# Performance work log

Measured on AMD Instinct MI355X. Metric: run time of the kernel, lower is better.

The kernel has to match this reference:

```python
import jax, jax.numpy as jnp
import numpy as np

NUM_HEADS = 16


def setup_inputs() -> dict:
    key = jax.random.key(0)
    k1, k2, k3 = jax.random.split(key, 3)
    B, N, C = 8, 1024, 1024
    x = jax.random.normal(k1, (B, N, C), dtype=jnp.float32)
    w_qkv = jax.random.normal(k2, (C, 3 * C), dtype=jnp.float32) * (C ** -0.5)
    w_proj = jax.random.normal(k3, (C, C), dtype=jnp.float32) * (C ** -0.5)
    b_proj = jnp.zeros((C,), dtype=jnp.float32)
    return {"x": x, "w_qkv": w_qkv, "w_proj": w_proj, "b_proj": b_proj}


def reference(x, w_qkv, w_proj, b_proj):
    B, N, C = x.shape
    H = NUM_HEADS
    hd = C // H
    scale = hd ** -0.5
    # qkv: [B,N,3C] -> [3,B,H,N,hd]
    qkv = (x @ w_qkv).reshape(B, N, 3, H, hd)
    qkv = jnp.transpose(qkv, (2, 0, 3, 1, 4))
    q, k, v = qkv[0], qkv[1], qkv[2]
    # attention scores [B,H,N,N], softmax over keys (attn_drop=0 in eval)
    attn = jax.nn.softmax(jnp.einsum('bhnd,bhmd->bhnm', q, k) * scale, axis=-1)
    # context -> [B,N,C]
    out = jnp.einsum('bhnm,bhmd->bnhd', attn, v).reshape(B, N, C)
    out = out @ w_proj + b_proj  # proj_drop=0 in eval
    return out, attn
```

## Files before the change

kernel.cpp:

```cpp
#include <hip/hip_runtime.h>


typedef unsigned short ushort_t;
typedef __bf16 bf16x8 __attribute__((ext_vector_type(8)));
typedef float floatx4 __attribute__((ext_vector_type(4)));

__device__ __forceinline__ ushort_t f2bf(float f) {
    __bf16 h = (__bf16)f;
    return *(ushort_t*)&h;
}

__global__ void transpose_f32_bf16(const float* __restrict__ in, ushort_t* __restrict__ out,
                                   int rows, int cols) {
    __shared__ ushort_t tile[32][33];
    int bx = blockIdx.x * 32;
    int by = blockIdx.y * 32;
    int tx = threadIdx.x;
    for (int i = threadIdx.y; i < 32; i += 8)
        tile[i][tx] = f2bf(in[(long)(by + i) * cols + bx + tx]);
    __syncthreads();
    for (int i = threadIdx.y; i < 32; i += 8)
        out[(long)(bx + i) * rows + by + tx] = tile[tx][i];
}

template <int AFP32>
__device__ __forceinline__ bf16x8 load_a8(const void* A_, long off) {
    if (AFP32) {
        const float* p = (const float*)A_ + off;
        floatx4 f0 = *(const floatx4*)p;
        floatx4 f1 = *(const floatx4*)(p + 4);
        bf16x8 r;
#pragma unroll
        for (int i = 0; i < 4; i++) { r[i] = (__bf16)f0[i]; r[i + 4] = (__bf16)f1[i]; }
        return r;
    } else {
        return *(const bf16x8*)((const ushort_t*)A_ + off);
    }
}

template <int MODE, int AFP32>
__global__ __launch_bounds__(256, 3)
void gemm_bt(const void* __restrict__ A, const ushort_t* __restrict__ Bt,
             int M, int Nc, int K,
             void* __restrict__ out_p, const float* __restrict__ bias) {
    __shared__ ushort_t As[128 * 32];
    __shared__ ushort_t Bs[128 * 32];
    const int tid  = threadIdx.x;
    const int wave = tid >> 6, lane = tid & 63;
    const int quad = lane >> 4, l16 = lane & 15;
    const int bm = blockIdx.y * 128, bn = blockIdx.x * 128;
    const int wm = (wave & 1) * 64, wn = (wave >> 1) * 64;

    floatx4 acc[4][4] = {};

    const int c0 = tid, c1 = tid + 256;
    const int row0 = c0 >> 2, kk0 = (c0 & 3) * 8;
    const int row1 = c1 >> 2, kk1 = (c1 & 3) * 8;

    for (int k0 = 0; k0 < K; k0 += 32) {
        bf16x8 a0 = load_a8<AFP32>(A, (long)(bm + row0) * K + k0 + kk0);
        bf16x8 a1 = load_a8<AFP32>(A, (long)(bm + row1) * K + k0 + kk1);
        bf16x8 b0 = *(const bf16x8*)(Bt + (long)(bn + row0) * K + k0 + kk0);
        bf16x8 b1 = *(const bf16x8*)(Bt + (long)(bn + row1) * K + k0 + kk1);
        __syncthreads();
        *(bf16x8*)&As[c0 * 8] = a0;
        *(bf16x8*)&As[c1 * 8] = a1;
        *(bf16x8*)&Bs[c0 * 8] = b0;
        *(bf16x8*)&Bs[c1 * 8] = b1;
        __syncthreads();
        bf16x8 af[4], bfr[4];
#pragma unroll
        for (int i = 0; i < 4; i++) {
            af[i]  = *(const bf16x8*)&As[(wm + i * 16 + l16) * 32 + quad * 8];
            bfr[i] = *(const bf16x8*)&Bs[(wn + i * 16 + l16) * 32 + quad * 8];
        }
#pragma unroll
        for (int mi = 0; mi < 4; mi++)
#pragma unroll
            for (int ni = 0; ni < 4; ni++)
                acc[mi][ni] = __builtin_amdgcn_mfma_f32_16x16x32_bf16(af[mi], bfr[ni], acc[mi][ni], 0, 0, 0);
    }

    if (MODE == 0) {
        ushort_t* qb  = (ushort_t*)out_p;
        ushort_t* kb  = qb + (size_t)8388608;
        ushort_t* vtb = qb + (size_t)16777216;
#pragma unroll
        for (int ni = 0; ni < 4; ni++) {
            int n = bn + wn + ni * 16 + l16;
            int t = n >> 10, c = n & 1023, h = c >> 6, d = c & 63;
#pragma unroll
            for (int mi = 0; mi < 4; mi++) {
                floatx4 v = acc[mi][ni];
#pragma unroll
                for (int r = 0; r < 4; r++) {
                    int m = bm + wm + mi * 16 + quad * 4 + r;
                    int b = m >> 10, tok = m & 1023;
                    long bh = (long)b * 16 + h;
                    ushort_t val = f2bf(v[r]);
                    if (t == 0)      qb[(bh * 1024 + tok) * 64 + d] = val;
                    else if (t == 1) kb[(bh * 1024 + tok) * 64 + d] = val;
                    else             vtb[(bh * 64 + d) * 1024 + tok] = val;
                }
            }
        }
    } else {
        float* outf = (float*)out_p;
#pragma unroll
        for (int ni = 0; ni < 4; ni++) {
            int n = bn + wn + ni * 16 + l16;
            float bv = bias[n];
#pragma unroll
            for (int mi = 0; mi < 4; mi++) {
                floatx4 v = acc[mi][ni];
#pragma unroll
                for (int r = 0; r < 4; r++) {
                    int m = bm + wm + mi * 16 + quad * 4 + r;
                    outf[(long)m * Nc + n] = v[r] + bv;
                }
            }
        }
    }
}

__global__ __launch_bounds__(256, 2)
void attn_fused(const ushort_t* __restrict__ q, const ushort_t* __restrict__ k,
                const ushort_t* __restrict__ vt, float* __restrict__ attn_out,
                ushort_t* __restrict__ ctx) {
    constexpr int SSTR = 1028;
    __shared__ float S[16 * SSTR];
    __shared__ float red_m[16];
    __shared__ float red_il[16];

    const int bh = blockIdx.x >> 6;
    const int qt = blockIdx.x & 63;
    const int qbase = qt * 16;
    const int tid = threadIdx.x;
    const int wave = tid >> 6, lane = tid & 63;
    const int quad = lane >> 4, l16 = lane & 15;

    const ushort_t* qrow = q + ((long)bh * 1024 + qbase + l16) * 64 + quad * 8;
    bf16x8 aq0 = *(const bf16x8*)(qrow);
    bf16x8 aq1 = *(const bf16x8*)(qrow + 32);

    const int key0 = wave * 256;
    const ushort_t* kp = k + ((long)bh * 1024 + key0 + l16) * 64 + quad * 8;
    bf16x8 bk0 = *(const bf16x8*)(kp);
    bf16x8 bk1 = *(const bf16x8*)(kp + 32);

    for (int kt = 0; kt < 16; kt++) {
        int ktn = (kt + 1 < 16) ? kt + 1 : 15;
        const ushort_t* npk = kp + (long)ktn * 1024;
        bf16x8 nb0 = *(const bf16x8*)(npk);
        bf16x8 nb1 = *(const bf16x8*)(npk + 32);
        floatx4 s4 = {0.f, 0.f, 0.f, 0.f};
        s4 = __builtin_amdgcn_mfma_f32_16x16x32_bf16(aq0, bk0, s4, 0, 0, 0);
        s4 = __builtin_amdgcn_mfma_f32_16x16x32_bf16(aq1, bk1, s4, 0, 0, 0);
        int keyc = key0 + kt * 16 + l16;
#pragma unroll
        for (int r = 0; r < 4; r++)
            S[(quad * 4 + r) * SSTR + keyc] = s4[r] * 0.125f;
        bk0 = nb0; bk1 = nb1;
    }
    __syncthreads();

    {
        int row = tid >> 4, sub = tid & 15;
        float m = -1e30f;
        for (int i = sub; i < 1024; i += 16) m = fmaxf(m, S[row * SSTR + i]);
#pragma unroll
        for (int o = 1; o < 16; o <<= 1) m = fmaxf(m, __shfl_xor(m, o, 64));
        float l = 0.f;
        for (int i = sub; i < 1024; i += 16) l += __expf(S[row * SSTR + i] - m);
#pragma unroll
        for (int o = 1; o < 16; o <<= 1) l += __shfl_xor(l, o, 64);
        if (sub == 0) { red_m[row] = m; red_il[row] = 1.0f / l; }
    }
    __syncthreads();

    float* aout = attn_out + ((long)bh * 1024 + qbase) * 1024;
    for (int idx = tid; idx < 16 * 256; idx += 256) {
        int r = idx >> 8, k4 = (idx & 255) * 4;
        float m = red_m[r], il = red_il[r];
        floatx4 pv;
#pragma unroll
        for (int j = 0; j < 4; j++) {
            float p = __expf(S[r * SSTR + k4 + j] - m) * il;
            S[r * SSTR + k4 + j] = p;
            pv[j] = p;
        }
        *(floatx4*)&aout[(long)r * 1024 + k4] = pv;
    }
    __syncthreads();

    floatx4 o4 = {0.f, 0.f, 0.f, 0.f};
    const ushort_t* vrow = vt + ((long)bh * 64 + wave * 16 + l16) * 1024 + quad * 8;
    for (int ks = 0; ks < 32; ks++) {
        const float* sp = &S[l16 * SSTR + ks * 32 + quad * 8];
        floatx4 p0 = *(const floatx4*)(sp);
        floatx4 p1 = *(const floatx4*)(sp + 4);
        bf16x8 pa;
#pragma unroll
        for (int i = 0; i < 4; i++) { pa[i] = (__bf16)p0[i]; pa[i + 4] = (__bf16)p1[i]; }
        bf16x8 vb = *(const bf16x8*)(vrow + ks * 32);
        o4 = __builtin_amdgcn_mfma_f32_16x16x32_bf16(pa, vb, o4, 0, 0, 0);
    }
    int b = bh >> 4, h = bh & 15;
    ushort_t* cp = ctx + ((long)b * 1024 + qbase) * 1024 + h * 64 + wave * 16 + l16;
#pragma unroll
    for (int r = 0; r < 4; r++)
        cp[(long)(quad * 4 + r) * 1024] = f2bf(o4[r]);
}

extern "C" void kernel_launch(void* const* d_in, const int* in_sizes, int n_in,
                              void* d_out, int out_size, void* d_ws, size_t ws_size,
                              hipStream_t stream) {
    const float* x      = (const float*)d_in[0];
    const float* w_qkv  = (const float*)d_in[1];
    const float* w_proj = (const float*)d_in[2];
    const float* b_proj = (const float*)d_in[3];

    float* out  = (float*)d_out;
    float* attn = out + (size_t)8 * 1024 * 1024;

    ushort_t* ws     = (ushort_t*)d_ws;
    ushort_t* q      = ws;
    ushort_t* kk     = ws + (size_t)8  * 1024 * 1024;
    ushort_t* vt     = ws + (size_t)16 * 1024 * 1024;
    ushort_t* ctx    = ws + (size_t)24 * 1024 * 1024;
    ushort_t* wqkvt  = ws + (size_t)32 * 1024 * 1024;
    ushort_t* wprojt = ws + (size_t)35 * 1024 * 1024;

    transpose_f32_bf16<<<dim3(96, 32), dim3(32, 8), 0, stream>>>(w_qkv, wqkvt, 1024, 3072);
    transpose_f32_bf16<<<dim3(32, 32), dim3(32, 8), 0, stream>>>(w_proj, wprojt, 1024, 1024);

    gemm_bt<0, 1><<<dim3(24, 64), dim3(256), 0, stream>>>(x, wqkvt, 8192, 3072, 1024, q, (const float*)nullptr);

    attn_fused<<<dim3(8192), dim3(256), 0, stream>>>(q, kk, vt, attn, ctx);

    gemm_bt<1, 0><<<dim3(8, 64), dim3(256), 0, stream>>>(ctx, wprojt, 8192, 1024, 1024, out, b_proj);
}
```

Baseline: 991.6 us.

## Keep attention scores in registers and stage probabilities as swizzled bf16 in LDS

The score tile now stays in registers, with the softmax max and sum computed through lane shuffles and a small cross-wave LDS reduction. This replaces the 64KB fp32 shared buffer and its multiple passes. Probabilities are written to LDS as bf16 with an XOR swizzle, which shrinks LDS use so the launch bound can rise to 3 blocks per SM. The catch is that the global attn stores become scalar per-lane writes instead of float4 vectors, and holding 16 floatx4 per lane raises register pressure.

```diff
diff --git a/kernel.cpp b/kernel.cpp
--- a/kernel.cpp
+++ b/kernel.cpp
@@ -123,14 +123,13 @@
     }
 }
 
-__global__ __launch_bounds__(256, 2)
+__global__ __launch_bounds__(256, 3)
 void attn_fused(const ushort_t* __restrict__ q, const ushort_t* __restrict__ k,
                 const ushort_t* __restrict__ vt, float* __restrict__ attn_out,
                 ushort_t* __restrict__ ctx) {
-    constexpr int SSTR = 1028;
-    __shared__ float S[16 * SSTR];
-    __shared__ float red_m[16];
-    __shared__ float red_il[16];
+    __shared__ ushort_t Sb[16 * 1024];
+    __shared__ float redm[4][16];
+    __shared__ float redl[4][16];
 
     const int bh = blockIdx.x >> 6;
     const int qt = blockIdx.x & 63;
@@ -145,63 +144,85 @@
 
     const int key0 = wave * 256;
     const ushort_t* kp = k + ((long)bh * 1024 + key0 + l16) * 64 + quad * 8;
-    bf16x8 bk0 = *(const bf16x8*)(kp);
-    bf16x8 bk1 = *(const bf16x8*)(kp + 32);
-
+
+    floatx4 s[16];
+#pragma unroll
     for (int kt = 0; kt < 16; kt++) {
-        int ktn = (kt + 1 < 16) ? kt + 1 : 15;
-        const ushort_t* npk = kp + (long)ktn * 1024;
-        bf16x8 nb0 = *(const bf16x8*)(npk);
-        bf16x8 nb1 = *(const bf16x8*)(npk + 32);
+        const ushort_t* kpp = kp + (long)kt * 1024;
+        bf16x8 bk0 = *(const bf16x8*)(kpp);
+        bf16x8 bk1 = *(const bf16x8*)(kpp + 32);
         floatx4 s4 = {0.f, 0.f, 0.f, 0.f};
         s4 = __builtin_amdgcn_mfma_f32_16x16x32_bf16(aq0, bk0, s4, 0, 0, 0);
         s4 = __builtin_amdgcn_mfma_f32_16x16x32_bf16(aq1, bk1, s4, 0, 0, 0);
-        int keyc = key0 + kt * 16 + l16;
-#pragma unroll
-        for (int r = 0; r < 4; r++)
-            S[(quad * 4 + r) * SSTR + keyc] = s4[r] * 0.125f;
-        bk0 = nb0; bk1 = nb1;
-    }
-    __syncthreads();
-
-    {
-        int row = tid >> 4, sub = tid & 15;
-        float m = -1e30f;
-        for (int i = sub; i < 1024; i += 16) m = fmaxf(m, S[row * SSTR + i]);
-#pragma unroll
-        for (int o = 1; o < 16; o <<= 1) m = fmaxf(m, __shfl_xor(m, o, 64));
+        s[kt] = s4;
+    }
+
+    float m4[4], l4[4];
+#pragma unroll
+    for (int r = 0; r < 4; r++) {
+        float m = s[0][r];
+#pragma unroll
+        for (int kt = 1; kt < 16; kt++) m = fmaxf(m, s[kt][r]);
+#pragma unroll
+        for (int o = 1; o < 16; o <<= 1) m = fmaxf(m, __shfl_xor(m, o, 16));
+        m4[r] = m;
+    }
+    if (l16 == 0) {
+#pragma unroll
+        for (int r = 0; r < 4; r++) redm[wave][quad * 4 + r] = m4[r];
+    }
+    __syncthreads();
+#pragma unroll
+    for (int r = 0; r < 4; r++) {
+        float m = redm[0][quad * 4 + r];
+#pragma unroll
+        for (int w = 1; w < 4; w++) m = fmaxf(m, redm[w][quad * 4 + r]);
+        m4[r] = m;
         float l = 0.f;
-        for (int i = sub; i < 1024; i += 16) l += __expf(S[row * SSTR + i] - m);
-#pragma unroll
-        for (int o = 1; o < 16; o <<= 1) l += __shfl_xor(l, o, 64);
-        if (sub == 0) { red_m[row] = m; red_il[row] = 1.0f / l; }
-    }
-    __syncthreads();
+#pragma unroll
+        for (int kt = 0; kt < 16; kt++) {
+            float p = __expf((s[kt][r] - m) * 0.125f);
+            s[kt][r] = p;
+            l += p;
+        }
+#pragma unroll
+        for (int o = 1; o < 16; o <<= 1) l += __shfl_xor(l, o, 16);
+        l4[r] = l;
+    }
+    if (l16 == 0) {
+#pragma unroll
+        for (int r = 0; r < 4; r++) redl[wave][quad * 4 + r] = l4[r];
+    }
+    __syncthreads();
+#pragma unroll
+    for (int r = 0; r < 4; r++) {
+        float l = redl[0][quad * 4 + r] + redl[1][quad * 4 + r]
+                + redl[2][quad * 4 + r] + redl[3][quad * 4 + r];
+        l4[r] = 1.0f / l;
+    }
 
     float* aout = attn_out + ((long)bh * 1024 + qbase) * 1024;
-    for (int idx = tid; idx < 16 * 256; idx += 256) {
-        int r = idx >> 8, k4 = (idx & 255) * 4;
-        float m = red_m[r], il = red_il[r];
-        floatx4 pv;
-#pragma unroll
-        for (int j = 0; j < 4; j++) {
-            float p = __expf(S[r * SSTR + k4 + j] - m) * il;
-            S[r * SSTR + k4 + j] = p;
-            pv[j] = p;
-        }
-        *(floatx4*)&aout[(long)r * 1024 + k4] = pv;
+#pragma unroll
+    for (int kt = 0; kt < 16; kt++) {
+        int key = key0 + kt * 16 + l16;
+#pragma unroll
+        for (int r = 0; r < 4; r++) {
+            int row = quad * 4 + r;
+            float p = s[kt][r] * l4[r];
+            aout[(long)row * 1024 + key] = p;
+            int byt = row * 2048 + ((key * 2) ^ ((row & 7) << 4));
+            *(ushort_t*)((char*)Sb + byt) = f2bf(p);
+        }
     }
     __syncthreads();
 
     floatx4 o4 = {0.f, 0.f, 0.f, 0.f};
     const ushort_t* vrow = vt + ((long)bh * 64 + wave * 16 + l16) * 1024 + quad * 8;
+    const char* sbrow = (const char*)Sb + l16 * 2048;
+    const int sxor = (l16 & 7) << 4;
+#pragma unroll 4
     for (int ks = 0; ks < 32; ks++) {
-        const float* sp = &S[l16 * SSTR + ks * 32 + quad * 8];
-        floatx4 p0 = *(const floatx4*)(sp);
-        floatx4 p1 = *(const floatx4*)(sp + 4);
-        bf16x8 pa;
-#pragma unroll
-        for (int i = 0; i < 4; i++) { pa[i] = (__bf16)p0[i]; pa[i + 4] = (__bf16)p1[i]; }
+        bf16x8 pa = *(const bf16x8*)(sbrow + ((ks * 64 + quad * 16) ^ sxor));
         bf16x8 vb = *(const bf16x8*)(vrow + ks * 32);
         o4 = __builtin_amdgcn_mfma_f32_16x16x32_bf16(pa, vb, o4, 0, 0, 0);
     }
```

Result: faster. 954.9 us (-3.7%).
